# Optimization experiments

Measured on AMD Instinct MI355X. Metric: run time of the kernel, lower is better.

The kernel has to match this reference:

```python
import jax, jax.numpy as jnp
import numpy as np

N = 100000
E = 1600000
D_IN = 64
HIDDEN = [64, 64]
D_OUT = 64


def _sage_layer(x, src, dst, Wl, bl, Wr):
    # gather source features, scatter-max into destination nodes
    agg = jax.ops.segment_max(x[src], dst, num_segments=x.shape[0])  # [N, d_in]
    agg = jnp.where(jnp.isfinite(agg), agg, jnp.zeros((), x.dtype))  # isolated nodes -> 0 (PyG fill)
    return agg @ Wl + bl + x @ Wr  # lin_l(aggr) + lin_r(x), bias only on lin_l


def setup_inputs() -> dict:
    key = jax.random.key(0)
    ks = jax.random.split(key, 12)
    x = jax.random.normal(ks[0], (N, D_IN), dtype=jnp.float32)
    edge_index = jax.random.randint(ks[1], (2, E), 0, N, dtype=jnp.int64)
    dims = [D_IN] + HIDDEN + [D_OUT]  # [64, 64, 64, 64]
    inp = {"x": x, "edge_index": edge_index}
    for i in range(3):
        din, dout = dims[i], dims[i + 1]
        s = 1.0 / np.sqrt(din)
        inp[f"Wl{i}"] = jax.random.uniform(ks[2 + 3 * i], (din, dout), jnp.float32, -s, s)
        inp[f"bl{i}"] = jax.random.uniform(ks[3 + 3 * i], (dout,), jnp.float32, -s, s)
        inp[f"Wr{i}"] = jax.random.uniform(ks[4 + 3 * i], (din, dout), jnp.float32, -s, s)
    return inp


def reference(x, edge_index, Wl0, bl0, Wr0, Wl1, bl1, Wr1, Wl2, bl2, Wr2):
    src, dst = edge_index[0], edge_index[1]
    # dropout p=0.0 -> identity; relu after every conv including the last
    h = jax.nn.relu(_sage_layer(x, src, dst, Wl0, bl0, Wr0))
    h = jax.nn.relu(_sage_layer(h, src, dst, Wl1, bl1, Wr1))
    h = jax.nn.relu(_sage_layer(h, src, dst, Wl2, bl2, Wr2))
    return h
```

## Files before the change

kernel.cpp:

```cpp
#include <hip/hip_runtime.h>
#include <math.h>

#define THREADS 256
#define CHUNK 4096
#define SLAB 4096

typedef __attribute__((ext_vector_type(8))) short bf16x8;
typedef __attribute__((ext_vector_type(4))) float f32x4;

__device__ __forceinline__ unsigned rne(float f) {
    unsigned b = __float_as_uint(f);
    return b + 0x7fffu + ((b >> 16) & 1u);
}

__device__ __forceinline__ unsigned enc_map(unsigned u) {
    return u ^ (((((u >> 15) & 0x00010001u) * 0xFFFFu)) | 0x80008000u);
}
__device__ __forceinline__ unsigned dec_map(unsigned e) {
    return e ^ ((((((~e) >> 15) & 0x00010001u) * 0xFFFFu)) | 0x80008000u);
}
#define ENC_NEG_INF 0x007F007Fu

__device__ __forceinline__ unsigned pkmax(unsigned a, unsigned b) {
    unsigned d;
    asm("v_pk_max_u16 %0, %1, %2" : "=v"(d) : "v"(a), "v"(b));
    return d;
}

__device__ __forceinline__ int detect64(const int* __restrict__ ei) {
    return ((ei[1] | ei[3] | ei[5] | ei[7] | ei[9] | ei[11]) == 0) ? 1 : 0;
}
__device__ __forceinline__ int get_src(const int* ei, int e, int i, int is64) {
    return is64 ? (int)((const long long*)ei)[i] : ei[i];
}
__device__ __forceinline__ int get_dst(const int* ei, int e, int i, int is64) {
    return is64 ? (int)((const long long*)ei)[e + i] : ei[e + i];
}

__global__ void k_zero_int(int* __restrict__ p, int n) {
    int i = blockIdx.x * blockDim.x + threadIdx.x;
    if (i < n) p[i] = 0;
}

__global__ __launch_bounds__(256) void k_cvtw(const float4* __restrict__ x4, uint2* __restrict__ hb, int n4,
                                              const float* __restrict__ Wl0, const float* __restrict__ Wr0,
                                              const float* __restrict__ Wl1, const float* __restrict__ Wr1,
                                              const float* __restrict__ Wl2, const float* __restrict__ Wr2,
                                              unsigned* __restrict__ wt0, unsigned* __restrict__ wt1,
                                              unsigned* __restrict__ wt2) {
    int i = blockIdx.x * 256 + threadIdx.x;
    if (i < n4) {
        float4 v = x4[i];
        unsigned p0 = (rne(v.x) >> 16) | (rne(v.y) & 0xffff0000u);
        unsigned p1 = (rne(v.z) >> 16) | (rne(v.w) & 0xffff0000u);
        hb[i] = make_uint2(enc_map(p0), enc_map(p1));
        return;
    }
    int id = i - n4;
    if (id < 3 * 4096) {
        int layer = id >> 12;
        int r = id & 4095;
        const float* Wl = (layer == 0) ? Wl0 : (layer == 1) ? Wl1 : Wl2;
        const float* Wr = (layer == 0) ? Wr0 : (layer == 1) ? Wr1 : Wr2;
        unsigned* wt = (layer == 0) ? wt0 : (layer == 1) ? wt1 : wt2;
        int nrow = r >> 6;
        int k2 = r & 63;
        const float* W = (k2 < 32) ? Wl : Wr;
        int k = (k2 < 32) ? (k2 * 2) : (k2 * 2 - 64);
        unsigned lo = rne(W[k * 64 + nrow]) >> 16;
        unsigned hi = rne(W[(k + 1) * 64 + nrow]) & 0xffff0000u;
        wt[nrow * 64 + k2] = lo | hi;
    }
}


__global__ __launch_bounds__(256) void k_bscatter(const int* __restrict__ ei, int e,
                                                  int* __restrict__ bucket_cur,
                                                  int* __restrict__ part, int nbuckets) {
    __shared__ int hist[1024];
    __shared__ int basev[1024];
    int t = threadIdx.x;
#pragma unroll
    for (int j = 0; j < 4; j++) hist[t + j * 256] = 0;
    __syncthreads();
    int is64 = detect64(ei);
    int base = blockIdx.x * CHUNK;
    int ds[16], ss[16];
#pragma unroll
    for (int it = 0; it < 16; it++) {
        int i = base + t + it * 256;
        ds[it] = -1;
        ss[it] = 0;
        if (i < e) {
            ds[it] = get_dst(ei, e, i, is64);
            ss[it] = get_src(ei, e, i, is64);
            atomicAdd(&hist[ds[it] >> 7], 1);
        }
    }
    __syncthreads();
#pragma unroll
    for (int j = 0; j < 4; j++) {
        int b = t + j * 256;
        if (b < nbuckets) {
            int c = hist[b];
            if (c) basev[b] = atomicAdd(&bucket_cur[b], c);
        }
    }
    __syncthreads();
#pragma unroll
    for (int it = 0; it < 16; it++) {
        if (ds[it] >= 0) {
            int bk = ds[it] >> 7;
            int pos = atomicAdd(&basev[bk], 1);
            pos = min(pos, SLAB - 1);
            part[bk * SLAB + pos] = (ss[it] << 7) | (ds[it] & 127);
        }
    }
}

__global__ __launch_bounds__(256) void k_bfinal(const int* __restrict__ part,
                                                const int* __restrict__ bucket_cnt,
                                                int* __restrict__ row_beg,
                                                int* __restrict__ row_end,
                                                int* __restrict__ col, int n) {
    __shared__ int deg[128], cur[128], sc[128];
    int b = blockIdx.x, t = threadIdx.x;
    int cnt = bucket_cnt[b];
    const int* slab = part + b * SLAB;
    int node0 = b << 7;
    if (t < 128) deg[t] = 0;
    __syncthreads();
    for (int i = t; i < cnt; i += 256) atomicAdd(&deg[slab[i] & 127], 1);
    __syncthreads();
    int v = (t < 128) ? deg[t] : 0;
    int dp = (v > 0) ? ((v + 7) & ~7) : 0;
    if (t < 128) sc[t] = dp;
    __syncthreads();
    for (int off = 1; off < 128; off <<= 1) {
        int u = (t < 128 && t >= off) ? sc[t - off] : 0;
        __syncthreads();
        if (t < 128) sc[t] += u;
        __syncthreads();
    }
    int base = b * SLAB;
    int beg = 0;
    if (t < 128) {
        beg = base + sc[t] - dp;
        int node = node0 + t;
        if (node < n) {
            row_beg[node] = beg;
            row_end[node] = beg + dp;
        }
        cur[t] = beg;
    }
    __syncthreads();
    for (int i = t; i < cnt; i += 256) {
        int p = slab[i];
        int pos = atomicAdd(&cur[p & 127], 1);
        col[pos] = p & ~127;
    }
    __syncthreads();
    if (t < 128 && v > 0) {
        int first = col[beg];
        for (int j = v; j < dp; j++) col[beg + j] = first;
    }
}

__global__ __launch_bounds__(512, 8) void k_fused(const unsigned* __restrict__ hin,
                                                  const int* __restrict__ row_beg,
                                                  const int* __restrict__ row_end,
                                                  const int* __restrict__ col,
                                                  const unsigned* __restrict__ Wt,
                                                  const float* __restrict__ bl,
                                                  float* __restrict__ outf,
                                                  unsigned* __restrict__ outb,
                                                  int n) {
    __shared__ char smem[17408 + 17408 + 256];
    short (*Abuf)[136] = (short(*)[136])smem;
    float (*Cs)[68] = (float(*)[68])smem;
    short (*Wts)[136] = (short(*)[136])(smem + 17408);
    float* bs = (float*)(smem + 34816);

    int t = threadIdx.x;
    int node0 = blockIdx.x * 64;

#pragma unroll
    for (int it = 0; it < 2; it++) {
        int c = t + it * 512;
        int nr = c >> 4, k16 = c & 15;
        uint4 w = *(const uint4*)(Wt + nr * 64 + k16 * 4);
        *(uint4*)&Wts[nr][k16 * 8] = w;
    }
    {
        int row = t >> 3, k8 = t & 7;
        int node = node0 + row;
        uint4 w = make_uint4(0, 0, 0, 0);
        if (node < n) {
            w = *(const uint4*)(hin + (size_t)node * 32 + k8 * 4);
            w.x = dec_map(w.x);
            w.y = dec_map(w.y);
            w.z = dec_map(w.z);
            w.w = dec_map(w.w);
        }
        *(uint4*)&Abuf[row][64 + k8 * 8] = w;
    }
    if (t < 64) bs[t] = bl[t];

    const char* hp = (const char*)hin;
    int off8 = (t & 15) << 3;
#pragma unroll
    for (int pass = 0; pass < 2; pass++) {
        int gl = pass * 32 + (t >> 4);
        int g = node0 + gl;
        uint2 res = make_uint2(0u, 0u);
        if (g < n) {
            int b = row_beg[g], e = row_end[g];
            if (b < e) {
                unsigned m0 = ENC_NEG_INF, m1 = ENC_NEG_INF;
                for (int k = b; k < e; k += 8) {
                    int4 c0 = *(const int4*)(col + k);
                    int4 c1 = *(const int4*)(col + k + 4);
                    uint2 r0 = *(const uint2*)(hp + (unsigned)(c0.x + off8));
                    uint2 r1 = *(const uint2*)(hp + (unsigned)(c0.y + off8));
                    uint2 r2 = *(const uint2*)(hp + (unsigned)(c0.z + off8));
                    uint2 r3 = *(const uint2*)(hp + (unsigned)(c0.w + off8));
                    uint2 r4 = *(const uint2*)(hp + (unsigned)(c1.x + off8));
                    uint2 r5 = *(const uint2*)(hp + (unsigned)(c1.y + off8));
                    uint2 r6 = *(const uint2*)(hp + (unsigned)(c1.z + off8));
                    uint2 r7 = *(const uint2*)(hp + (unsigned)(c1.w + off8));
                    unsigned a0 = pkmax(pkmax(r0.x, r1.x), pkmax(r2.x, r3.x));
                    unsigned a1 = pkmax(pkmax(r4.x, r5.x), pkmax(r6.x, r7.x));
                    unsigned b0 = pkmax(pkmax(r0.y, r1.y), pkmax(r2.y, r3.y));
                    unsigned b1 = pkmax(pkmax(r4.y, r5.y), pkmax(r6.y, r7.y));
                    m0 = pkmax(m0, pkmax(a0, a1));
                    m1 = pkmax(m1, pkmax(b0, b1));
                }
                res = make_uint2(dec_map(m0), dec_map(m1));
            }
        }
        *(uint2*)&Abuf[gl][(t & 15) * 4] = res;
    }
    __syncthreads();

    int lane = t & 63;
    int wv = t >> 6;
    int r0 = (wv & 3) * 16;
    int c0 = (wv >> 2) * 32;
    int lr = lane & 15, lk = lane >> 4;

    f32x4 acc0 = {0.f, 0.f, 0.f, 0.f}, acc1 = acc0;
#pragma unroll
    for (int kk = 0; kk < 4; kk++) {
        int ko = kk * 32 + lk * 8;
        bf16x8 a = *(const bf16x8*)&Abuf[r0 + lr][ko];
        bf16x8 b0 = *(const bf16x8*)&Wts[c0 + lr][ko];
        bf16x8 b1 = *(const bf16x8*)&Wts[c0 + 16 + lr][ko];
        acc0 = __builtin_amdgcn_mfma_f32_16x16x32_bf16(a, b0, acc0, 0, 0, 0);
        acc1 = __builtin_amdgcn_mfma_f32_16x16x32_bf16(a, b1, acc1, 0, 0, 0);
    }
    __syncthreads();
#pragma unroll
    for (int reg = 0; reg < 4; reg++) {
        int row = r0 + lk * 4 + reg;
        Cs[row][c0 + lr] = acc0[reg];
        Cs[row][c0 + 16 + lr] = acc1[reg];
    }
    __syncthreads();

#pragma unroll
    for (int it = 0; it < 2; it++) {
        int idx = t + it * 512;
        int row = idx >> 4, qc = idx & 15;
        int node = node0 + row;
        if (node < n) {
            float4 v = *(float4*)&Cs[row][qc * 4];
            float4 bb = *(float4*)&bs[qc * 4];
            float4 o;
            o.x = fmaxf(v.x + bb.x, 0.f);
            o.y = fmaxf(v.y + bb.y, 0.f);
            o.z = fmaxf(v.z + bb.z, 0.f);
            o.w = fmaxf(v.w + bb.w, 0.f);
            if (outf) *(float4*)(outf + (size_t)node * 64 + qc * 4) = o;
            if (outb) {
                unsigned p0 = (rne(o.x) >> 16) | (rne(o.y) & 0xffff0000u);
                unsigned p1 = (rne(o.z) >> 16) | (rne(o.w) & 0xffff0000u);
                *(uint2*)(outb + (size_t)node * 32 + qc * 2) = make_uint2(enc_map(p0), enc_map(p1));
            }
        }
    }
}


extern "C" void kernel_launch(void* const* d_in, const int* in_sizes, int n_in,
                              void* d_out, int out_size, void* d_ws, size_t ws_size,
                              hipStream_t stream) {
    const float* x = (const float*)d_in[0];
    const int* ei = (const int*)d_in[1];
    const float* Wl0 = (const float*)d_in[2];
    const float* bl0 = (const float*)d_in[3];
    const float* Wr0 = (const float*)d_in[4];
    const float* Wl1 = (const float*)d_in[5];
    const float* bl1 = (const float*)d_in[6];
    const float* Wr1 = (const float*)d_in[7];
    const float* Wl2 = (const float*)d_in[8];
    const float* bl2 = (const float*)d_in[9];
    const float* Wr2 = (const float*)d_in[10];

    int n = in_sizes[0] / 64;
    int e = in_sizes[1] / 2;
    int nbuckets = (n + 127) >> 7;

    char* p = (char*)d_ws;
    auto alloc = [&](size_t bytes) {
        void* q = (void*)p;
        p += (bytes + 255) & ~(size_t)255;
        return q;
    };
    int* bucket_cur = (int*)alloc((size_t)nbuckets * 4);
    int* row_beg = (int*)alloc((size_t)n * 4);
    int* row_end = (int*)alloc((size_t)n * 4);
    int* col = (int*)alloc((size_t)nbuckets * SLAB * 4);
    int* part = (int*)alloc((size_t)nbuckets * SLAB * 4);
    unsigned* hb0 = (unsigned*)alloc((size_t)n * 64 * 2);
    unsigned* hb1 = (unsigned*)alloc((size_t)n * 64 * 2);
    unsigned* wt0 = (unsigned*)alloc(64 * 64 * 4);
    unsigned* wt1 = (unsigned*)alloc(64 * 64 * 4);
    unsigned* wt2 = (unsigned*)alloc(64 * 64 * 4);

    float* out = (float*)d_out;

    int gb_chunk = (e + CHUNK - 1) / CHUNK;
    int gb_fused = (n + 63) / 64;
    int n4 = n * 16;
    int gb_cvtw = (n4 + 3 * 4096 + THREADS - 1) / THREADS;

    k_zero_int<<<(nbuckets + THREADS - 1) / THREADS, THREADS, 0, stream>>>(bucket_cur, nbuckets);
    k_bscatter<<<gb_chunk, 256, 0, stream>>>(ei, e, bucket_cur, part, nbuckets);
    k_bfinal<<<nbuckets, 256, 0, stream>>>(part, bucket_cur, row_beg, row_end, col, n);

    k_cvtw<<<gb_cvtw, THREADS, 0, stream>>>((const float4*)x, (uint2*)hb0, n4,
                                            Wl0, Wr0, Wl1, Wr1, Wl2, Wr2, wt0, wt1, wt2);

    k_fused<<<gb_fused, 512, 0, stream>>>(hb0, row_beg, row_end, col, wt0, bl0, (float*)nullptr, hb1, n);
    k_fused<<<gb_fused, 512, 0, stream>>>(hb1, row_beg, row_end, col, wt1, bl1, (float*)nullptr, hb0, n);
    k_fused<<<gb_fused, 512, 0, stream>>>(hb0, row_beg, row_end, col, wt2, bl2, out, (unsigned*)nullptr, n);
}
```

Before: 157.1 us.

## Interleave two node gathers per thread and fold bucket zeroing into conversion kernel

The gather loop in the fused SAGE kernel now processes both of a thread's destination nodes in the same loop iteration instead of in two sequential passes. This doubles the independent loads in flight to hide gather latency. Lengths are clamped so the shorter row re-reads its last 8-edge window, and slab tails are zero-padded so over-reads land on valid indices. The separate bucket-counter zeroing kernel is merged into the input/weight conversion kernel, saving one launch. Unequal degrees add some redundant loads for the shorter row.

After: 155.2 us. No clear change (-1.2%).

```diff
diff --git a/kernel.cpp b/kernel.cpp
--- a/kernel.cpp
+++ b/kernel.cpp
@@ -35,11 +35,6 @@
 }
 __device__ __forceinline__ int get_dst(const int* ei, int e, int i, int is64) {
     return is64 ? (int)((const long long*)ei)[e + i] : ei[e + i];
-}
-
-__global__ void k_zero_int(int* __restrict__ p, int n) {
-    int i = blockIdx.x * blockDim.x + threadIdx.x;
-    if (i < n) p[i] = 0;
 }
 
 __global__ __launch_bounds__(256) void k_cvtw(const float4* __restrict__ x4, uint2* __restrict__ hb, int n4,
@@ -47,7 +42,8 @@
                                               const float* __restrict__ Wl1, const float* __restrict__ Wr1,
                                               const float* __restrict__ Wl2, const float* __restrict__ Wr2,
                                               unsigned* __restrict__ wt0, unsigned* __restrict__ wt1,
-                                              unsigned* __restrict__ wt2) {
+                                              unsigned* __restrict__ wt2,
+                                              int* __restrict__ bucket_cur, int nbuckets) {
     int i = blockIdx.x * 256 + threadIdx.x;
     if (i < n4) {
         float4 v = x4[i];
@@ -70,7 +66,10 @@
         unsigned lo = rne(W[k * 64 + nrow]) >> 16;
         unsigned hi = rne(W[(k + 1) * 64 + nrow]) & 0xffff0000u;
         wt[nrow * 64 + k2] = lo | hi;
-    }
+        return;
+    }
+    id -= 3 * 4096;
+    if (id < nbuckets) bucket_cur[id] = 0;
 }
 
 
@@ -163,6 +162,12 @@
     if (t < 128 && v > 0) {
         int first = col[beg];
         for (int j = v; j < dp; j++) col[beg + j] = first;
+    }
+    if (t == 0) {
+        int total = sc[127];
+#pragma unroll
+        for (int j = 0; j < 8; j++)
+            if (total + j < SLAB) col[base + total + j] = 0;
     }
 }
 
@@ -208,62 +213,82 @@
 
     const char* hp = (const char*)hin;
     int off8 = (t & 15) << 3;
-#pragma unroll
-    for (int pass = 0; pass < 2; pass++) {
-        int gl = pass * 32 + (t >> 4);
-        int g = node0 + gl;
-        uint2 res = make_uint2(0u, 0u);
-        if (g < n) {
-            int b = row_beg[g], e = row_end[g];
-            if (b < e) {
-                unsigned m0 = ENC_NEG_INF, m1 = ENC_NEG_INF;
-                for (int k = b; k < e; k += 8) {
-                    int4 c0 = *(const int4*)(col + k);
-                    int4 c1 = *(const int4*)(col + k + 4);
-                    uint2 r0 = *(const uint2*)(hp + (unsigned)(c0.x + off8));
-                    uint2 r1 = *(const uint2*)(hp + (unsigned)(c0.y + off8));
-                    uint2 r2 = *(const uint2*)(hp + (unsigned)(c0.z + off8));
-                    uint2 r3 = *(const uint2*)(hp + (unsigned)(c0.w + off8));
-                    uint2 r4 = *(const uint2*)(hp + (unsigned)(c1.x + off8));
-                    uint2 r5 = *(const uint2*)(hp + (unsigned)(c1.y + off8));
-                    uint2 r6 = *(const uint2*)(hp + (unsigned)(c1.z + off8));
-                    uint2 r7 = *(const uint2*)(hp + (unsigned)(c1.w + off8));
-                    unsigned a0 = pkmax(pkmax(r0.x, r1.x), pkmax(r2.x, r3.x));
-                    unsigned a1 = pkmax(pkmax(r4.x, r5.x), pkmax(r6.x, r7.x));
-                    unsigned b0 = pkmax(pkmax(r0.y, r1.y), pkmax(r2.y, r3.y));
-                    unsigned b1 = pkmax(pkmax(r4.y, r5.y), pkmax(r6.y, r7.y));
-                    m0 = pkmax(m0, pkmax(a0, a1));
-                    m1 = pkmax(m1, pkmax(b0, b1));
-                }
-                res = make_uint2(dec_map(m0), dec_map(m1));
-            }
-        }
-        *(uint2*)&Abuf[gl][(t & 15) * 4] = res;
+    {
+        int gl0 = t >> 4;
+        int gl1 = gl0 + 32;
+        int g0 = node0 + gl0, g1 = node0 + gl1;
+        int gs0 = min(g0, n - 1), gs1 = min(g1, n - 1);
+        int b0 = row_beg[gs0], e0 = row_end[gs0];
+        int b1 = row_beg[gs1], e1 = row_end[gs1];
+        int n0 = e0 - b0, n1 = e1 - b1;
+        bool z0 = (g0 >= n) || (n0 == 0);
+        bool z1 = (g1 >= n) || (n1 == 0);
+        int last0 = z0 ? 0 : n0 - 8;
+        int last1 = z1 ? 0 : n1 - 8;
+        int nt = max(z0 ? 0 : n0, z1 ? 0 : n1);
+        unsigned m0a = ENC_NEG_INF, m0b = ENC_NEG_INF;
+        unsigned m1a = ENC_NEG_INF, m1b = ENC_NEG_INF;
+        for (int k = 0; k < nt; k += 8) {
+            int k0 = b0 + min(k, last0);
+            int k1 = b1 + min(k, last1);
+            int4 c00 = *(const int4*)(col + k0);
+            int4 c01 = *(const int4*)(col + k0 + 4);
+            int4 c10 = *(const int4*)(col + k1);
+            int4 c11 = *(const int4*)(col + k1 + 4);
+            uint2 r0 = *(const uint2*)(hp + (unsigned)(c00.x + off8));
+            uint2 r1 = *(const uint2*)(hp + (unsigned)(c00.y + off8));
+            uint2 r2 = *(const uint2*)(hp + (unsigned)(c00.z + off8));
+            uint2 r3 = *(const uint2*)(hp + (unsigned)(c00.w + off8));
+            uint2 r4 = *(const uint2*)(hp + (unsigned)(c01.x + off8));
+            uint2 r5 = *(const uint2*)(hp + (unsigned)(c01.y + off8));
+            uint2 r6 = *(const uint2*)(hp + (unsigned)(c01.z + off8));
+            uint2 r7 = *(const uint2*)(hp + (unsigned)(c01.w + off8));
+            uint2 s0 = *(const uint2*)(hp + (unsigned)(c10.x + off8));
+            uint2 s1 = *(const uint2*)(hp + (unsigned)(c10.y + off8));
+            uint2 s2 = *(const uint2*)(hp + (unsigned)(c10.z + off8));
+            uint2 s3 = *(const uint2*)(hp + (unsigned)(c10.w + off8));
+            uint2 s4 = *(const uint2*)(hp + (unsigned)(c11.x + off8));
+            uint2 s5 = *(const uint2*)(hp + (unsigned)(c11.y + off8));
+            uint2 s6 = *(const uint2*)(hp + (unsigned)(c11.z + off8));
+            uint2 s7 = *(const uint2*)(hp + (unsigned)(c11.w + off8));
+            m0a = pkmax(m0a, pkmax(pkmax(pkmax(r0.x, r1.x), pkmax(r2.x, r3.x)),
+                                   pkmax(pkmax(r4.x, r5.x), pkmax(r6.x, r7.x))));
+            m0b = pkmax(m0b, pkmax(pkmax(pkmax(r0.y, r1.y), pkmax(r2.y, r3.y)),
+                                   pkmax(pkmax(r4.y, r5.y), pkmax(r6.y, r7.y))));
+            m1a = pkmax(m1a, pkmax(pkmax(pkmax(s0.x, s1.x), pkmax(s2.x, s3.x)),
+                                   pkmax(pkmax(s4.x, s5.x), pkmax(s6.x, s7.x))));
+            m1b = pkmax(m1b, pkmax(pkmax(pkmax(s0.y, s1.y), pkmax(s2.y, s3.y)),
+                                   pkmax(pkmax(s4.y, s5.y), pkmax(s6.y, s7.y))));
+        }
+        uint2 res0 = z0 ? make_uint2(0u, 0u) : make_uint2(dec_map(m0a), dec_map(m0b));
+        uint2 res1 = z1 ? make_uint2(0u, 0u) : make_uint2(dec_map(m1a), dec_map(m1b));
+        *(uint2*)&Abuf[gl0][(t & 15) * 4] = res0;
+        *(uint2*)&Abuf[gl1][(t & 15) * 4] = res1;
     }
     __syncthreads();
 
     int lane = t & 63;
     int wv = t >> 6;
-    int r0 = (wv & 3) * 16;
-    int c0 = (wv >> 2) * 32;
+    int r0_ = (wv & 3) * 16;
+    int c0_ = (wv >> 2) * 32;
     int lr = lane & 15, lk = lane >> 4;
 
     f32x4 acc0 = {0.f, 0.f, 0.f, 0.f}, acc1 = acc0;
 #pragma unroll
     for (int kk = 0; kk < 4; kk++) {
         int ko = kk * 32 + lk * 8;
-        bf16x8 a = *(const bf16x8*)&Abuf[r0 + lr][ko];
-        bf16x8 b0 = *(const bf16x8*)&Wts[c0 + lr][ko];
-        bf16x8 b1 = *(const bf16x8*)&Wts[c0 + 16 + lr][ko];
+        bf16x8 a = *(const bf16x8*)&Abuf[r0_ + lr][ko];
+        bf16x8 b0 = *(const bf16x8*)&Wts[c0_ + lr][ko];
+        bf16x8 b1 = *(const bf16x8*)&Wts[c0_ + 16 + lr][ko];
         acc0 = __builtin_amdgcn_mfma_f32_16x16x32_bf16(a, b0, acc0, 0, 0, 0);
         acc1 = __builtin_amdgcn_mfma_f32_16x16x32_bf16(a, b1, acc1, 0, 0, 0);
     }
     __syncthreads();
 #pragma unroll
     for (int reg = 0; reg < 4; reg++) {
-        int row = r0 + lk * 4 + reg;
-        Cs[row][c0 + lr] = acc0[reg];
-        Cs[row][c0 + 16 + lr] = acc1[reg];
+        int row = r0_ + lk * 4 + reg;
+        Cs[row][c0_ + lr] = acc0[reg];
+        Cs[row][c0_ + 16 + lr] = acc1[reg];
     }
     __syncthreads();
 
@@ -332,14 +357,14 @@
     int gb_chunk = (e + CHUNK - 1) / CHUNK;
     int gb_fused = (n + 63) / 64;
     int n4 = n * 16;
-    int gb_cvtw = (n4 + 3 * 4096 + THREADS - 1) / THREADS;
-
-    k_zero_int<<<(nbuckets + THREADS - 1) / THREADS, THREADS, 0, stream>>>(bucket_cur, nbuckets);
+    int gb_cvtw = (n4 + 3 * 4096 + nbuckets + THREADS - 1) / THREADS;
+
+    k_cvtw<<<gb_cvtw, THREADS, 0, stream>>>((const float4*)x, (uint2*)hb0, n4,
+                                            Wl0, Wr0, Wl1, Wr1, Wl2, Wr2, wt0, wt1, wt2,
+                                            bucket_cur, nbuckets);
+
     k_bscatter<<<gb_chunk, 256, 0, stream>>>(ei, e, bucket_cur, part, nbuckets);
     k_bfinal<<<nbuckets, 256, 0, stream>>>(part, bucket_cur, row_beg, row_end, col, n);
-
-    k_cvtw<<<gb_cvtw, THREADS, 0, stream>>>((const float4*)x, (uint2*)hb0, n4,
-                                            Wl0, Wr0, Wl1, Wr1, Wl2, Wr2, wt0, wt1, wt2);
 
     k_fused<<<gb_fused, 512, 0, stream>>>(hb0, row_beg, row_end, col, wt0, bl0, (float*)nullptr, hb1, n);
     k_fused<<<gb_fused, 512, 0, stream>>>(hb1, row_beg, row_end, col, wt1, bl1, (float*)nullptr, hb0, n);
```
